# Optimization experiments

Hardware: AMD Instinct MI355X
Metric: run time of the kernel (lower is better)

## Reference

```python
import jax, jax.numpy as jnp
import numpy as np

PS = 5    # patch_w for rgb arch
K = 14    # num nearest neighbors
WS = 29   # search window side


def _patchify(img_pad, H, W):
    """img_pad: [t, H+2*(whalf+phalf), W+..., c] channels-last.
    Returns patch features over the search grid: [t, H+2*whalf, W+2*whalf, PS*PS*c]."""
    whalf = WS // 2
    Hg, Wg = H + 2 * whalf, W + 2 * whalf
    slices = [img_pad[:, dy:dy + Hg, dx:dx + Wg, :]
              for dy in range(PS) for dx in range(PS)]
    return jnp.concatenate(slices, axis=-1)


def _forward(noisy, sigma):
    t, c, H, W = noisy.shape
    # rescale to [-1,1] and remove per-frame channel means (as in forward)
    x = (noisy / 255.0 - 0.5) / 0.5
    means = x.mean((-2, -1), keepdims=True)
    x = x - means
    xl = jnp.transpose(x, (0, 2, 3, 1))  # [t,H,W,c]

    phalf, whalf = PS // 2, WS // 2
    pad = phalf + whalf
    xp = jnp.pad(xl, ((0, 0), (pad, pad), (pad, pad), (0, 0)), mode='reflect')

    P = _patchify(xp, H, W)              # [t, H+2*whalf, W+2*whalf, D]
    D = PS * PS * c
    Pq = P[:, whalf:whalf + H, whalf:whalf + W, :]  # query patches [t,H,W,D]

    # --- windowed kNN patch search: scan over WS*WS offsets ---
    def dist_step(_, o):
        oy, ox = o // WS, o % WS
        Pn = jax.lax.dynamic_slice(P, (0, oy, ox, 0), (t, H, W, D))
        d = jnp.sum((Pq - Pn) ** 2, axis=-1)  # [t,H,W]
        return None, d

    _, dists = jax.lax.scan(dist_step, None, jnp.arange(WS * WS))
    dists = jnp.transpose(dists, (1, 2, 3, 0))  # [t,H,W,WS*WS]

    negv, idx = jax.lax.top_k(-dists, K)        # k smallest distances
    dk = -negv                                   # [t,H,W,K]
    oy, ox = idx // WS, idx % WS

    # --- gather neighbor patches ---
    rows = jnp.arange(H)[None, :, None, None] + oy   # [t,H,W,K]
    cols = jnp.arange(W)[None, None, :, None] + ox
    ti = jnp.arange(t)[:, None, None, None]
    neigh = P[ti, rows, cols]                        # [t,H,W,K,D]

    # --- patch denoise: distance-softmax weighted neighbor aggregation ---
    sig = (jnp.float32(sigma) / 255.0) / 0.5
    beta = 1.0 / (2.0 * sig * sig * D)
    wts = jax.nn.softmax(-beta * dk, axis=-1)        # [t,H,W,K]
    pdeno = jnp.einsum('thwk,thwkd->thwd', wts, neigh)  # [t,H,W,D]
    patches = pdeno.reshape(t, H, W, PS, PS, c)

    # --- weighted iFold: overlap-add + count normalization ---
    acc = jnp.zeros((t, H + 2 * phalf, W + 2 * phalf, c), x.dtype)
    cnt = jnp.zeros((t, H + 2 * phalf, W + 2 * phalf, 1), x.dtype)
    ones = jnp.ones((t, H, W, 1), x.dtype)
    for py in range(PS):
        for px in range(PS):
            acc = acc.at[:, py:py + H, px:px + W, :].add(patches[:, :, :, py, px, :])
            cnt = cnt.at[:, py:py + H, px:px + W, :].add(ones)
    deno = acc / cnt
    deno = deno[:, phalf:H + phalf, phalf:W + phalf, :]  # final_format crop

    deno = jnp.transpose(deno, (0, 3, 1, 2)) + means
    deno = 255.0 * (deno * 0.5 + 0.5)
    return deno


def setup_inputs() -> dict:
    key = jax.random.key(0)
    k1, _ = jax.random.split(key)
    noisy = jax.random.uniform(k1, (4, 3, 128, 128), dtype=jnp.float32) * 255.0
    sigma = 25
    return {"noisy": noisy, "sigma": sigma}


def reference(noisy, sigma):
    return _forward(noisy, sigma)
```

## Files before the change

kernel.cpp:

```cpp
#include <hip/hip_runtime.h>

#define T_ 4
#define H_ 128
#define W_ 128
#define XPS 160
#define WSZ 29
#define K_ 14
#define ACCS 132

#define SROWS 4
#define SCOLS 12
#define TR 36
#define RS 136
#define NBI 32
#define NBJ 11
#define NW 4
#define OPW 211

#define HS 40
#define N2S 40

#define DPP_SHL(x, n) __uint_as_float((unsigned)__builtin_amdgcn_update_dpp( \
        0, (int)__float_as_uint(x), 0x100 + (n), 0xF, 0xF, true))

#define SORTED_INSERT(s, key)                                        \
    do {                                                             \
        _Pragma("unroll")                                            \
        for (int _i = K_ - 1; _i >= 1; _i--)                         \
            s[_i] = min(max(key, s[_i - 1]), s[_i]);                 \
        s[0] = min(s[0], key);                                       \
    } while (0)

__global__ void k_means(const float* __restrict__ noisy, float* __restrict__ means) {
    int tc = blockIdx.x;
    const float* src = noisy + (size_t)tc * (H_ * W_);
    float s = 0.f;
    for (int i = threadIdx.x; i < H_ * W_; i += 256) s += src[i];
    __shared__ float red[256];
    red[threadIdx.x] = s;
    __syncthreads();
    for (int st = 128; st > 0; st >>= 1) {
        if ((int)threadIdx.x < st) red[threadIdx.x] += red[threadIdx.x + st];
        __syncthreads();
    }
    if (threadIdx.x == 0)
        means[tc] = red[0] * (1.f / (H_ * W_)) * (2.f / 255.f) - 1.f;
}

__global__ void k_pad(const float* __restrict__ noisy, const float* __restrict__ means,
                      float* __restrict__ xp) {
    int idx = blockIdx.x * 256 + threadIdx.x;
    if (idx >= T_ * XPS * XPS) return;
    int t  = idx / (XPS * XPS);
    int rr = (idx / XPS) % XPS;
    int cc = idx % XPS;
    int ry = rr - 16; if (ry < 0) ry = -ry; if (ry > H_ - 1) ry = 2 * (H_ - 1) - ry;
    int rx = cc - 16; if (rx < 0) rx = -rx; if (rx > W_ - 1) rx = 2 * (W_ - 1) - rx;
    float* dst = xp + (size_t)idx * 3;
#pragma unroll
    for (int c = 0; c < 3; c++) {
        float v = noisy[(((size_t)t * 3 + c) * H_ + ry) * W_ + rx];
        dst[c] = v * (2.f / 255.f) - 1.f - means[t * 3 + c];
    }
}

__global__ __launch_bounds__(256, 4)
void k_main(const float* __restrict__ xp, const int* __restrict__ sigma_p,
            float* __restrict__ acc) {
    __shared__ __align__(16) float tileF[TR * RS];
    __shared__ unsigned kbuf[NW * K_][49];
    __shared__ float N2s[32 * N2S];

    const int tid = threadIdx.x;
    const int b   = blockIdx.x;
    const int t   = b / (NBI * NBJ);
    const int rem = b % (NBI * NBJ);
    const int bi  = (rem / NBJ) * SROWS;
    const int bj  = (rem % NBJ) * SCOLS;

    const float* src = xp + ((size_t)(t * XPS + bi) * XPS + bj) * 3;
    for (int i = tid; i < TR * 33; i += 256) {
        int rr = i / 33, q = i - rr * 33;
        float4 v = *reinterpret_cast<const float4*>(src + (size_t)rr * (XPS * 3) + q * 4);
        *reinterpret_cast<float4*>(&tileF[rr * RS + q * 4]) = v;
    }
    __syncthreads();

    float* hbuf = reinterpret_cast<float*>(&kbuf[0][0]);
    for (int i = tid; i < TR * HS; i += 256) {
        int r = i / HS, c = i - (i / HS) * HS;
        const float* tp = &tileF[r * RS + c * 3];
        float s = 0.f;
#pragma unroll
        for (int d = 0; d < 15; d++) { float v = tp[d]; s = fmaf(v, v, s); }
        hbuf[i] = s;
    }
    __syncthreads();

    for (int i = tid; i < 32 * HS; i += 256) {
        int r = i / HS, c = i - (i / HS) * HS;
        const float* hp = &hbuf[r * HS + c];
        N2s[r * N2S + c] = hp[0] + hp[HS] + hp[2 * HS] + hp[3 * HS] + hp[4 * HS];
    }
    __syncthreads();

    const int w    = tid >> 6;
    const int lane = tid & 63;
    const int g    = lane >> 4;
    const int tj   = lane & 15;
    const bool valid = (tj < SCOLS) && (bj + tj < W_);

    float A[5][3];
#pragma unroll
    for (int dy = 0; dy < 5; dy++)
#pragma unroll
        for (int c = 0; c < 3; c++)
            A[dy][c] = tileF[(14 + g + dy) * RS + (14 + tj) * 3 + c];
    const float N2q = N2s[(g + 14) * N2S + (tj + 14)];

    unsigned s[K_];
#pragma unroll
    for (int k = 0; k < K_; k++) s[k] = 0xFFFFFF00u + k;

    const int oy0 = (w == 0) ? 0 : 8 + 7 * (w - 1);
    const int oy1 = (w == 0) ? 8 : 8 + 7 * w;
    for (int oy = oy0; oy < oy1; oy++) {
        const float* bp = &tileF[(g + oy) * RS + tj * 3];
        const float* np = &N2s[(g + oy) * N2S + tj];
        int o = oy * WSZ;
        for (int ox = 0; ox < WSZ; ox++, o++, bp += 3, np++) {
            float c0 = 0.f, c1 = 0.f, c2 = 0.f;
#pragma unroll
            for (int dy = 0; dy < 5; dy++) {
                c0 = fmaf(A[dy][0], bp[dy * RS + 0], c0);
                c1 = fmaf(A[dy][1], bp[dy * RS + 1], c1);
                c2 = fmaf(A[dy][2], bp[dy * RS + 2], c2);
            }
            float cb = (c0 + c1) + c2;
            float a2 = cb + DPP_SHL(cb, 1);
            float a4 = a2 + DPP_SHL(a2, 2);
            float CB = a4 + DPP_SHL(cb, 4);
            float D = fmaf(-2.f, CB, N2q + np[0]);
            D = fmaxf(D, 0.f);
            unsigned key = (__float_as_uint(D) & 0xFFFFFC00u) | (unsigned)o;
            SORTED_INSERT(s, key);
        }
    }

    __syncthreads();
    const int pxi = g * SCOLS + tj;
    if (valid) {
#pragma unroll
        for (int k = 0; k < K_; k++) kbuf[w * K_ + k][pxi] = s[k];
    }
#pragma unroll
    for (int k = 0; k < K_; k++) s[k] = 0xFFFFFF00u + k;
    __syncthreads();

    if (valid) {
        for (int j = 0; j < NW * K_; j++) {
            unsigned key = kbuf[j][pxi];
            SORTED_INSERT(s, key);
        }
    }

    float sig  = (float)sigma_p[0] * (2.f / 255.f);
    float beta = 1.f / (2.f * sig * sig * 75.f);
    float wk[K_];
    int oyk[K_], oxk[K_];
    const float dmin = __uint_as_float(s[0] & 0xFFFFFC00u);
#pragma unroll
    for (int k = 0; k < K_; k++) {
        wk[k] = __uint_as_float(s[k] & 0xFFFFFC00u);
        int ok = (int)(s[k] & 1023u);
        oyk[k] = ok / WSZ;
        oxk[k] = ok - oyk[k] * WSZ;
    }
    float sw = 0.f;
#pragma unroll
    for (int k = 0; k < K_; k++) { float e = __expf(beta * (dmin - wk[k])); wk[k] = e; sw += e; }
    float inv = 1.f / sw;
#pragma unroll
    for (int k = 0; k < K_; k++) wk[k] *= inv;

    __syncthreads();
    float* accb = reinterpret_cast<float*>(&kbuf[0][0]);
    for (int i = tid; i < 8 * 16 * 3; i += 256) accb[i] = 0.f;
    __syncthreads();

    for (int p = w; p < 25; p += NW) {
        int py = p / 5, px = p - py * 5;
        if (valid) {
            float s0 = 0.f, s1 = 0.f, s2 = 0.f;
#pragma unroll
            for (int k = 0; k < K_; k++) {
                const float* nb = &tileF[(g + oyk[k] + py) * RS + (tj + oxk[k] + px) * 3];
                s0 += wk[k] * nb[0];
                s1 += wk[k] * nb[1];
                s2 += wk[k] * nb[2];
            }
            float* ap = accb + ((g + py) * 16 + (tj + px)) * 3;
            atomicAdd(ap + 0, s0);
            atomicAdd(ap + 1, s1);
            atomicAdd(ap + 2, s2);
        }
    }
    __syncthreads();

    for (int i = tid; i < 8 * 16 * 3; i += 256) {
        int ch = i % 3;
        int cc = (i / 3) & 15;
        int rr = i / 48;
        int gr = bi + rr, gc = bj + cc;
        if (gc < ACCS)
            atomicAdd(&acc[(((size_t)t * ACCS + gr) * ACCS + gc) * 3 + ch], accb[i]);
    }
}

__global__ void k_final(const float* __restrict__ acc, const float* __restrict__ means,
                        float* __restrict__ out) {
    int idx = blockIdx.x * 256 + threadIdx.x;
    if (idx >= T_ * 3 * H_ * W_) return;
    int j  = idx & 127;
    int i  = (idx >> 7) & 127;
    int ch = (idx >> 14) % 3;
    int t  = idx / (3 * H_ * W_);
    int r = i + 2, s = j + 2;
    int ny = (r < 4 ? r : 4) - (r > 127 ? r - 127 : 0) + 1;
    int nx = (s < 4 ? s : 4) - (s > 127 ? s - 127 : 0) + 1;
    float v = acc[(((size_t)t * ACCS + r) * ACCS + s) * 3 + ch] / (float)(ny * nx);
    v += means[t * 3 + ch];
    out[idx] = 127.5f * v + 127.5f;
}

extern "C" void kernel_launch(void* const* d_in, const int* in_sizes, int n_in,
                              void* d_out, int out_size, void* d_ws, size_t ws_size,
                              hipStream_t stream) {
    (void)in_sizes; (void)n_in; (void)out_size; (void)ws_size;
    const float* noisy = (const float*)d_in[0];
    const int*   sigma = (const int*)d_in[1];

    float* means = (float*)d_ws;
    float* xp    = means + 64;
    float* acc   = xp + (size_t)T_ * XPS * XPS * 3;
    float* out   = (float*)d_out;

    hipLaunchKernelGGL(k_means, dim3(12), dim3(256), 0, stream, noisy, means);
    hipLaunchKernelGGL(k_pad, dim3((T_ * XPS * XPS + 255) / 256), dim3(256), 0, stream,
                       noisy, means, xp);
    hipMemsetAsync(acc, 0, (size_t)T_ * ACCS * ACCS * 3 * sizeof(float), stream);
    hipLaunchKernelGGL(k_main, dim3(T_ * NBI * NBJ), dim3(256), 0, stream, xp, sigma, acc);
    hipLaunchKernelGGL(k_final, dim3((T_ * 3 * H_ * W_ + 255) / 256), dim3(256), 0, stream,
                       acc, means, out);
}
```

Before: 299.1 us.

## Split window search across eight wavefronts per block with early-exit merge

Doubles the k_main block to 512 threads so eight wavefronts each scan 3-4 offset rows of the search window, instead of four wavefronts scanning 7-8 rows. This cuts the serial search length per wave and the tail work per block. The merge step now stops reading a wave's sorted list once a key is no worse than the current 14th best. Shared memory is overlaid, with hbuf, N2s and accb all aliasing kbuf, to keep LDS usage down as the buffers grow. The cost is a longer merge across more lists, higher register pressure under launch_bounds(512,6), and data-dependent branching in the merge.

```diff
diff --git a/kernel.cpp b/kernel.cpp
--- a/kernel.cpp
+++ b/kernel.cpp
@@ -14,8 +14,8 @@
 #define RS 136
 #define NBI 32
 #define NBJ 11
-#define NW 4
-#define OPW 211
+#define NW 8
+#define NT 512
 
 #define HS 40
 #define N2S 40
@@ -64,12 +64,14 @@
     }
 }
 
-__global__ __launch_bounds__(256, 4)
+__global__ __launch_bounds__(NT, 6)
 void k_main(const float* __restrict__ xp, const int* __restrict__ sigma_p,
             float* __restrict__ acc) {
     __shared__ __align__(16) float tileF[TR * RS];
-    __shared__ unsigned kbuf[NW * K_][49];
-    __shared__ float N2s[32 * N2S];
+    __shared__ __align__(16) unsigned kbuf[NW * K_][49];
+    float* hbuf = reinterpret_cast<float*>(&kbuf[0][0]);
+    float* N2s  = reinterpret_cast<float*>(&kbuf[0][0]) + 1440;
+    float* accb = reinterpret_cast<float*>(&kbuf[0][0]);
 
     const int tid = threadIdx.x;
     const int b   = blockIdx.x;
@@ -79,28 +81,28 @@
     const int bj  = (rem % NBJ) * SCOLS;
 
     const float* src = xp + ((size_t)(t * XPS + bi) * XPS + bj) * 3;
-    for (int i = tid; i < TR * 33; i += 256) {
+    for (int i = tid; i < TR * 33; i += NT) {
         int rr = i / 33, q = i - rr * 33;
         float4 v = *reinterpret_cast<const float4*>(src + (size_t)rr * (XPS * 3) + q * 4);
         *reinterpret_cast<float4*>(&tileF[rr * RS + q * 4]) = v;
     }
     __syncthreads();
 
-    float* hbuf = reinterpret_cast<float*>(&kbuf[0][0]);
-    for (int i = tid; i < TR * HS; i += 256) {
+    for (int i = tid; i < TR * HS; i += NT) {
         int r = i / HS, c = i - (i / HS) * HS;
-        const float* tp = &tileF[r * RS + c * 3];
+        int tb = r * RS + c * 3;
         float s = 0.f;
 #pragma unroll
-        for (int d = 0; d < 15; d++) { float v = tp[d]; s = fmaf(v, v, s); }
+        for (int d = 0; d < 15; d++) { float v = tileF[tb + d]; s = fmaf(v, v, s); }
         hbuf[i] = s;
     }
     __syncthreads();
 
-    for (int i = tid; i < 32 * HS; i += 256) {
+    for (int i = tid; i < 32 * HS; i += NT) {
         int r = i / HS, c = i - (i / HS) * HS;
-        const float* hp = &hbuf[r * HS + c];
-        N2s[r * N2S + c] = hp[0] + hp[HS] + hp[2 * HS] + hp[3 * HS] + hp[4 * HS];
+        int hb = r * HS + c;
+        N2s[r * N2S + c] = hbuf[hb] + hbuf[hb + HS] + hbuf[hb + 2 * HS] +
+                           hbuf[hb + 3 * HS] + hbuf[hb + 4 * HS];
     }
     __syncthreads();
 
@@ -110,37 +112,39 @@
     const int tj   = lane & 15;
     const bool valid = (tj < SCOLS) && (bj + tj < W_);
 
+    const int qb = (14 + g) * RS + (14 + tj) * 3;
     float A[5][3];
 #pragma unroll
     for (int dy = 0; dy < 5; dy++)
 #pragma unroll
         for (int c = 0; c < 3; c++)
-            A[dy][c] = tileF[(14 + g + dy) * RS + (14 + tj) * 3 + c];
+            A[dy][c] = tileF[qb + dy * RS + c];
     const float N2q = N2s[(g + 14) * N2S + (tj + 14)];
 
     unsigned s[K_];
 #pragma unroll
     for (int k = 0; k < K_; k++) s[k] = 0xFFFFFF00u + k;
 
-    const int oy0 = (w == 0) ? 0 : 8 + 7 * (w - 1);
-    const int oy1 = (w == 0) ? 8 : 8 + 7 * w;
-    for (int oy = oy0; oy < oy1; oy++) {
-        const float* bp = &tileF[(g + oy) * RS + tj * 3];
-        const float* np = &N2s[(g + oy) * N2S + tj];
-        int o = oy * WSZ;
-        for (int ox = 0; ox < WSZ; ox++, o++, bp += 3, np++) {
+    const int oy0  = (w < 5) ? 4 * w : 20 + 3 * (w - 5);
+    const int nrow = (w < 5) ? 4 : 3;
+    for (int r = 0; r < nrow; r++) {
+        const int oy = oy0 + r;
+        int tb = (g + oy) * RS + tj * 3;
+        int nb = (g + oy) * N2S + tj;
+        int o  = oy * WSZ;
+        for (int ox = 0; ox < WSZ; ox++, o++, tb += 3, nb++) {
             float c0 = 0.f, c1 = 0.f, c2 = 0.f;
 #pragma unroll
             for (int dy = 0; dy < 5; dy++) {
-                c0 = fmaf(A[dy][0], bp[dy * RS + 0], c0);
-                c1 = fmaf(A[dy][1], bp[dy * RS + 1], c1);
-                c2 = fmaf(A[dy][2], bp[dy * RS + 2], c2);
+                c0 = fmaf(A[dy][0], tileF[tb + dy * RS + 0], c0);
+                c1 = fmaf(A[dy][1], tileF[tb + dy * RS + 1], c1);
+                c2 = fmaf(A[dy][2], tileF[tb + dy * RS + 2], c2);
             }
             float cb = (c0 + c1) + c2;
             float a2 = cb + DPP_SHL(cb, 1);
             float a4 = a2 + DPP_SHL(a2, 2);
             float CB = a4 + DPP_SHL(cb, 4);
-            float D = fmaf(-2.f, CB, N2q + np[0]);
+            float D = fmaf(-2.f, CB, N2q + N2s[nb]);
             D = fmaxf(D, 0.f);
             unsigned key = (__float_as_uint(D) & 0xFFFFFC00u) | (unsigned)o;
             SORTED_INSERT(s, key);
@@ -158,9 +162,12 @@
     __syncthreads();
 
     if (valid) {
-        for (int j = 0; j < NW * K_; j++) {
-            unsigned key = kbuf[j][pxi];
-            SORTED_INSERT(s, key);
+        for (int jw = 0; jw < NW; jw++) {
+            for (int k2 = 0; k2 < K_; k2++) {
+                unsigned key = kbuf[jw * K_ + k2][pxi];
+                if (key >= s[K_ - 1]) break;
+                SORTED_INSERT(s, key);
+            }
         }
     }
 
@@ -184,8 +191,7 @@
     for (int k = 0; k < K_; k++) wk[k] *= inv;
 
     __syncthreads();
-    float* accb = reinterpret_cast<float*>(&kbuf[0][0]);
-    for (int i = tid; i < 8 * 16 * 3; i += 256) accb[i] = 0.f;
+    for (int i = tid; i < 8 * 16 * 3; i += NT) accb[i] = 0.f;
     __syncthreads();
 
     for (int p = w; p < 25; p += NW) {
@@ -194,10 +200,10 @@
             float s0 = 0.f, s1 = 0.f, s2 = 0.f;
 #pragma unroll
             for (int k = 0; k < K_; k++) {
-                const float* nb = &tileF[(g + oyk[k] + py) * RS + (tj + oxk[k] + px) * 3];
-                s0 += wk[k] * nb[0];
-                s1 += wk[k] * nb[1];
-                s2 += wk[k] * nb[2];
+                int nbx = (g + oyk[k] + py) * RS + (tj + oxk[k] + px) * 3;
+                s0 += wk[k] * tileF[nbx + 0];
+                s1 += wk[k] * tileF[nbx + 1];
+                s2 += wk[k] * tileF[nbx + 2];
             }
             float* ap = accb + ((g + py) * 16 + (tj + px)) * 3;
             atomicAdd(ap + 0, s0);
@@ -207,7 +213,7 @@
     }
     __syncthreads();
 
-    for (int i = tid; i < 8 * 16 * 3; i += 256) {
+    for (int i = tid; i < 8 * 16 * 3; i += NT) {
         int ch = i % 3;
         int cc = (i / 3) & 15;
         int rr = i / 48;
@@ -249,7 +255,7 @@
     hipLaunchKernelGGL(k_pad, dim3((T_ * XPS * XPS + 255) / 256), dim3(256), 0, stream,
                        noisy, means, xp);
     hipMemsetAsync(acc, 0, (size_t)T_ * ACCS * ACCS * 3 * sizeof(float), stream);
-    hipLaunchKernelGGL(k_main, dim3(T_ * NBI * NBJ), dim3(256), 0, stream, xp, sigma, acc);
+    hipLaunchKernelGGL(k_main, dim3(T_ * NBI * NBJ), dim3(NT), 0, stream, xp, sigma, acc);
     hipLaunchKernelGGL(k_final, dim3((T_ * 3 * H_ * W_ + 255) / 256), dim3(256), 0, stream,
                        acc, means, out);
 }
```

Measured after the change: 302.4 us. No clear change (+1.1%).
